# Kernel optimization log

Measured on AMD Instinct MI355X. Metric: run time of the kernel, lower is better.

Reference implementation:

```python
import jax, jax.numpy as jnp
import numpy as np

DIM = 512
HEADS = 8
DIM_HEAD = 64
INNER = HEADS * DIM_HEAD  # 512
EPS = 1e-6


def setup_inputs() -> dict:
    key = jax.random.key(0)
    ks = jax.random.split(key, 6)
    B, N = 8, 2048
    x = jax.random.normal(ks[0], (B, N, DIM), dtype=jnp.float32)
    # nn.Linear stores weight as [out, in]; we keep that layout and transpose in matmul.
    w_qkv = jax.random.normal(ks[1], (3 * INNER, DIM), dtype=jnp.float32) * (1.0 / np.sqrt(DIM))
    w_proj = jax.random.normal(ks[2], (DIM, INNER), dtype=jnp.float32) * (1.0 / np.sqrt(INNER))
    b_proj = jax.random.normal(ks[3], (DIM,), dtype=jnp.float32) * 0.01
    ln_gamma = jnp.ones((DIM,), dtype=jnp.float32)
    ln_beta = jnp.zeros((DIM,), dtype=jnp.float32)
    return {"x": x, "w_qkv": w_qkv, "w_proj": w_proj, "b_proj": b_proj,
            "ln_gamma": ln_gamma, "ln_beta": ln_beta}


def reference(x, w_qkv, w_proj, b_proj, ln_gamma, ln_beta):
    B, N, D = x.shape
    H, Dh = HEADS, DIM_HEAD
    # LayerNorm (eps=1e-6)
    mu = jnp.mean(x, axis=-1, keepdims=True)
    var = jnp.mean(jnp.square(x - mu), axis=-1, keepdims=True)
    xn = (x - mu) * jax.lax.rsqrt(var + EPS) * ln_gamma + ln_beta
    # QKV projection (no bias)
    qkv = xn @ w_qkv.T  # [B, N, 3*INNER]
    q, k, v = jnp.split(qkv, 3, axis=-1)
    # [B, N, H, Dh] -> [B, H, N, Dh]
    q = q.reshape(B, N, H, Dh).transpose(0, 2, 1, 3)
    k = k.reshape(B, N, H, Dh).transpose(0, 2, 1, 3)
    v = v.reshape(B, N, H, Dh).transpose(0, 2, 1, 3)
    scale = Dh ** (-0.5)
    attn = jnp.einsum('bhnd,bhmd->bhnm', q, k) * scale  # [B, H, N, N]
    attn = jax.nn.softmax(attn, axis=-1)
    out = jnp.einsum('bhnm,bhmd->bhnd', attn, v)  # [B, H, N, Dh]
    out = out.transpose(0, 2, 1, 3).reshape(B, N, H * Dh)
    out = out @ w_proj.T + b_proj
    return out
```

## Files before the change

kernel.cpp:

```cpp
#include <hip/hip_runtime.h>

typedef unsigned short u16;
typedef __bf16 bf16x8 __attribute__((ext_vector_type(8)));
typedef float f32x4 __attribute__((ext_vector_type(4)));

#define DIMD 512
#define SEQN 2048
#define NB   8
#define NH   8
#define DH   64
#define BHN  (NB*NH)
#define MROWS (NB*SEQN)
#define QSCALE 0.18033688f

__device__ __forceinline__ u16 f2bf(float f) {
  union { float f; unsigned u; } x; x.f = f;
  unsigned r = x.u + 0x7fffu + ((x.u >> 16) & 1u);
  return (u16)(r >> 16);
}
__device__ __forceinline__ u16 f2bf_fast(float f) {
  union { float f; unsigned u; } x; x.f = f;
  return (u16)((x.u + 0x8000u) >> 16);
}

__device__ __forceinline__ void gll16(const u16* g, u16* lbase) {
#if __has_builtin(__builtin_amdgcn_global_load_lds)
  __builtin_amdgcn_global_load_lds(
      (const __attribute__((address_space(1))) unsigned int*)g,
      (__attribute__((address_space(3))) unsigned int*)lbase, 16, 0, 0);
#else
  *(uint4*)((u16*)lbase + (threadIdx.x & 63) * 8) = *(const uint4*)g;
#endif
}

__global__ __launch_bounds__(256) void wcvt(const float* __restrict__ w,
                                            u16* __restrict__ o, int n) {
  int i = (blockIdx.x * 256 + threadIdx.x) * 8;
  if (i >= n) return;
  float4 f0 = *(const float4*)(w + i);
  float4 f1 = *(const float4*)(w + i + 4);
  union { uint4 v; u16 s[8]; } u;
  u.s[0] = f2bf(f0.x); u.s[1] = f2bf(f0.y); u.s[2] = f2bf(f0.z); u.s[3] = f2bf(f0.w);
  u.s[4] = f2bf(f1.x); u.s[5] = f2bf(f1.y); u.s[6] = f2bf(f1.z); u.s[7] = f2bf(f1.w);
  *(uint4*)(o + i) = u.v;
}

__global__ __launch_bounds__(256) void ln_kernel(
    const float* __restrict__ x, const float* __restrict__ gamma,
    const float* __restrict__ beta, u16* __restrict__ xn) {
  int row = blockIdx.x * 4 + (threadIdx.x >> 6);
  int lane = threadIdx.x & 63;
  const float* xr = x + (size_t)row * DIMD;
  float f[8], g[8], b[8];
  *(float4*)&f[0] = *(const float4*)(xr + lane * 8);
  *(float4*)&f[4] = *(const float4*)(xr + lane * 8 + 4);
  *(float4*)&g[0] = *(const float4*)(gamma + lane * 8);
  *(float4*)&g[4] = *(const float4*)(gamma + lane * 8 + 4);
  *(float4*)&b[0] = *(const float4*)(beta + lane * 8);
  *(float4*)&b[4] = *(const float4*)(beta + lane * 8 + 4);
  float sum = 0.f, sq = 0.f;
#pragma unroll
  for (int i = 0; i < 8; ++i) { sum += f[i]; sq += f[i] * f[i]; }
#pragma unroll
  for (int off = 1; off < 64; off <<= 1) {
    sum += __shfl_xor(sum, off, 64);
    sq  += __shfl_xor(sq, off, 64);
  }
  float mean = sum * (1.0f / DIMD);
  float var = sq * (1.0f / DIMD) - mean * mean;
  float rstd = rsqrtf(var + 1e-6f);
  union { uint4 v; u16 s[8]; } uo;
#pragma unroll
  for (int i = 0; i < 8; ++i)
    uo.s[i] = f2bf((f[i] - mean) * rstd * g[i] + b[i]);
  *(uint4*)(xn + (size_t)row * DIMD + lane * 8) = uo.v;
}

__global__ __launch_bounds__(256) void qkv_gemm(
    const u16* __restrict__ A, const u16* __restrict__ Bm,
    u16* __restrict__ qo, u16* __restrict__ ko, u16* __restrict__ vto) {
  __shared__ __align__(16) u16 la[128 * 32];
  __shared__ __align__(16) u16 lb[128 * 32];
  const int K = DIMD;
  int tid = threadIdx.x;
  int bm = blockIdx.x, bn = blockIdx.y;
  int wid = tid >> 6, lane = tid & 63, lm = lane & 15, quad = lane >> 4;
  int wm = wid >> 1, wn = wid & 1;
  f32x4 acc[4][4] = {};
  const u16* Ab = A + (size_t)(bm * 128) * K;
  const u16* Bb = Bm + (size_t)(bn * 128) * K;
  int srow = (lane >> 2), scol = (lane & 3) * 8;
  for (int k0 = 0; k0 < K; k0 += 32) {
    __syncthreads();
#pragma unroll
    for (int r = 0; r < 2; ++r) {
      int seg = wid * 2 + r;
      int row = seg * 16 + srow;
      gll16(Ab + (size_t)row * K + k0 + scol, &la[seg * 512]);
      gll16(Bb + (size_t)row * K + k0 + scol, &lb[seg * 512]);
    }
    __syncthreads();
    bf16x8 af[4], bfr[4];
#pragma unroll
    for (int i = 0; i < 4; ++i)
      af[i] = *(const bf16x8*)&la[(wm * 64 + i * 16 + lm) * 32 + quad * 8];
#pragma unroll
    for (int j = 0; j < 4; ++j)
      bfr[j] = *(const bf16x8*)&lb[(wn * 64 + j * 16 + lm) * 32 + quad * 8];
#pragma unroll
    for (int i = 0; i < 4; ++i)
#pragma unroll
      for (int j = 0; j < 4; ++j)
        acc[i][j] = __builtin_amdgcn_mfma_f32_16x16x32_bf16(af[i], bfr[j], acc[i][j], 0, 0, 0);
  }
#pragma unroll
  for (int i = 0; i < 4; ++i) {
#pragma unroll
    for (int j = 0; j < 4; ++j) {
      int col = bn * 128 + wn * 64 + j * 16 + lm;
      int part = col >> 9, rem = col & 511;
      int h = rem >> 6, d = rem & 63;
      float sc = (part == 0) ? QSCALE : 1.0f;
#pragma unroll
      for (int r = 0; r < 4; ++r) {
        int rg = bm * 128 + wm * 64 + i * 16 + quad * 4 + r;
        int b = rg >> 11, nn = rg & 2047;
        int bh = b * NH + h;
        u16 val = f2bf(acc[i][j][r] * sc);
        if (part == 0)      qo[((size_t)bh * SEQN + nn) * DH + d] = val;
        else if (part == 1) ko[((size_t)bh * SEQN + nn) * DH + d] = val;
        else                vto[((size_t)bh * DH + d) * SEQN + nn] = val;
      }
    }
  }
}

__global__ __launch_bounds__(256, 4) void attn_kernel(
    const u16* __restrict__ q, const u16* __restrict__ k,
    const u16* __restrict__ vt, u16* __restrict__ att) {
  __shared__ __align__(16) u16 kt[64 * 64];
  __shared__ __align__(16) u16 vtt[64 * 64];
  __shared__ __align__(16) u16 plds[4 * 2 * 1152];
  int bh = blockIdx.x;
  int wid = threadIdx.x >> 6, lane = threadIdx.x & 63;
  int lm = lane & 15, quad = lane >> 4;
  int qrow0 = blockIdx.y * 128 + wid * 32;
  const u16* qb = q + (size_t)bh * SEQN * DH;
  const u16* kb = k + (size_t)bh * SEQN * DH;
  const u16* vb = vt + (size_t)bh * DH * SEQN;

  int cb_row = lane >> 3, cb_sub = lane & 7;
  int xsw = quad ^ (lm & 7);

  bf16x8 qf[2][2];
#pragma unroll
  for (int g = 0; g < 2; ++g)
#pragma unroll
    for (int c = 0; c < 2; ++c)
      qf[g][c] = *(const bf16x8*)(qb + (size_t)(qrow0 + g * 16 + lm) * DH + c * 32 + quad * 8);

  f32x4 Ot[2][4] = {};
  f32x4 lv[2] = {};

  for (int j0 = 0; j0 < SEQN; j0 += 64) {
    __syncthreads();
    if (wid < 2) {
#pragma unroll
      for (int i = 0; i < 4; ++i) {
        int rbase = wid * 32 + i * 8;
        int row = rbase + cb_row;
        int sc = ((cb_sub ^ (row & 7)) * 8);
        gll16(kb + (size_t)(j0 + row) * DH + sc, &kt[(wid * 256 + i * 64) * 8]);
      }
    } else {
#pragma unroll
      for (int i = 0; i < 4; ++i) {
        int rbase = (wid - 2) * 32 + i * 8;
        int row = rbase + cb_row;
        int sc = ((cb_sub ^ (row & 7)) * 8);
        gll16(vb + (size_t)row * SEQN + j0 + sc, &vtt[((wid - 2) * 256 + i * 64) * 8]);
      }
    }
    __syncthreads();

    bf16x8 kf[4][2];
#pragma unroll
    for (int js = 0; js < 4; ++js) {
      int row = js * 16 + lm;
      kf[js][0] = *(const bf16x8*)&kt[row * 64 + xsw * 8];
      kf[js][1] = *(const bf16x8*)&kt[row * 64 + (xsw ^ 4) * 8];
    }
    bf16x8 pa[2][2];
#pragma unroll
    for (int g = 0; g < 2; ++g) {
      u16* pg = plds + (wid * 2 + g) * 1152;
#pragma unroll
      for (int js = 0; js < 4; ++js) {
        f32x4 z = {0.f, 0.f, 0.f, 0.f};
        z = __builtin_amdgcn_mfma_f32_16x16x32_bf16(kf[js][0], qf[g][0], z, 0, 0, 0);
        z = __builtin_amdgcn_mfma_f32_16x16x32_bf16(kf[js][1], qf[g][1], z, 0, 0, 0);
        union { unsigned long long ll; u16 s4[4]; } pk;
#pragma unroll
        for (int r = 0; r < 4; ++r) {
          float p = __builtin_amdgcn_exp2f(z[r]);
          lv[g][r] += p;
          pk.s4[r] = f2bf_fast(p);
        }
        *(unsigned long long*)&pg[lm * 72 + js * 16 + quad * 4] = pk.ll;
      }
      pa[g][0] = *(const bf16x8*)&pg[lm * 72 + quad * 8];
      pa[g][1] = *(const bf16x8*)&pg[lm * 72 + 32 + quad * 8];
    }
#pragma unroll
    for (int db = 0; db < 4; ++db) {
      int row = db * 16 + lm;
      bf16x8 va0 = *(const bf16x8*)&vtt[row * 64 + xsw * 8];
      bf16x8 va1 = *(const bf16x8*)&vtt[row * 64 + (xsw ^ 4) * 8];
      Ot[0][db] = __builtin_amdgcn_mfma_f32_16x16x32_bf16(va0, pa[0][0], Ot[0][db], 0, 0, 0);
      Ot[0][db] = __builtin_amdgcn_mfma_f32_16x16x32_bf16(va1, pa[0][1], Ot[0][db], 0, 0, 0);
      Ot[1][db] = __builtin_amdgcn_mfma_f32_16x16x32_bf16(va0, pa[1][0], Ot[1][db], 0, 0, 0);
      Ot[1][db] = __builtin_amdgcn_mfma_f32_16x16x32_bf16(va1, pa[1][1], Ot[1][db], 0, 0, 0);
    }
  }
  int b = bh >> 3, h = bh & 7;
#pragma unroll
  for (int g = 0; g < 2; ++g) {
    float rs = (lv[g][0] + lv[g][1]) + (lv[g][2] + lv[g][3]);
    rs += __shfl_xor(rs, 16, 64);
    rs += __shfl_xor(rs, 32, 64);
    float inv = 1.0f / rs;
    size_t rowoff = ((size_t)(b * SEQN + qrow0 + g * 16 + lm)) * DIMD + h * DH;
#pragma unroll
    for (int db = 0; db < 4; ++db) {
      union { unsigned long long ll; u16 s4[4]; } ok;
#pragma unroll
      for (int r = 0; r < 4; ++r) ok.s4[r] = f2bf(Ot[g][db][r] * inv);
      *(unsigned long long*)&att[rowoff + db * 16 + quad * 4] = ok.ll;
    }
  }
}

__global__ __launch_bounds__(256) void proj_gemm(
    const u16* __restrict__ A, const u16* __restrict__ Bm,
    const float* __restrict__ bias, float* __restrict__ C) {
  __shared__ __align__(16) u16 la[128 * 32];
  __shared__ __align__(16) u16 lb[128 * 32];
  const int K = DIMD, N = DIMD;
  int tid = threadIdx.x;
  int bm = blockIdx.x, bn = blockIdx.y;
  int wid = tid >> 6, lane = tid & 63, lm = lane & 15, quad = lane >> 4;
  int wm = wid >> 1, wn = wid & 1;
  f32x4 acc[4][4] = {};
  const u16* Ab = A + (size_t)(bm * 128) * K;
  const u16* Bb = Bm + (size_t)(bn * 128) * K;
  int srow = (lane >> 2), scol = (lane & 3) * 8;
  for (int k0 = 0; k0 < K; k0 += 32) {
    __syncthreads();
#pragma unroll
    for (int r = 0; r < 2; ++r) {
      int seg = wid * 2 + r;
      int row = seg * 16 + srow;
      gll16(Ab + (size_t)row * K + k0 + scol, &la[seg * 512]);
      gll16(Bb + (size_t)row * K + k0 + scol, &lb[seg * 512]);
    }
    __syncthreads();
    bf16x8 af[4], bfr[4];
#pragma unroll
    for (int i = 0; i < 4; ++i)
      af[i] = *(const bf16x8*)&la[(wm * 64 + i * 16 + lm) * 32 + quad * 8];
#pragma unroll
    for (int j = 0; j < 4; ++j)
      bfr[j] = *(const bf16x8*)&lb[(wn * 64 + j * 16 + lm) * 32 + quad * 8];
#pragma unroll
    for (int i = 0; i < 4; ++i)
#pragma unroll
      for (int j = 0; j < 4; ++j)
        acc[i][j] = __builtin_amdgcn_mfma_f32_16x16x32_bf16(af[i], bfr[j], acc[i][j], 0, 0, 0);
  }
#pragma unroll
  for (int i = 0; i < 4; ++i)
#pragma unroll
    for (int j = 0; j < 4; ++j) {
      int col = bn * 128 + wn * 64 + j * 16 + lm;
      float bv = bias[col];
#pragma unroll
      for (int r = 0; r < 4; ++r) {
        int rg = bm * 128 + wm * 64 + i * 16 + quad * 4 + r;
        C[(size_t)rg * N + col] = acc[i][j][r] + bv;
      }
    }
}

extern "C" void kernel_launch(void* const* d_in, const int* in_sizes, int n_in,
                              void* d_out, int out_size, void* d_ws, size_t ws_size,
                              hipStream_t stream) {
  const float* x      = (const float*)d_in[0];
  const float* w_qkv  = (const float*)d_in[1];
  const float* w_proj = (const float*)d_in[2];
  const float* b_proj = (const float*)d_in[3];
  const float* gamma  = (const float*)d_in[4];
  const float* beta   = (const float*)d_in[5];
  float* out = (float*)d_out;

  const size_t SZ = (size_t)MROWS * DIMD;
  u16* xn  = (u16*)d_ws;
  u16* q   = xn + SZ;
  u16* kk  = q + SZ;
  u16* vt  = kk + SZ;
  u16* wqb = vt + SZ;
  u16* wpb = wqb + (size_t)3 * DIMD * DIMD;
  u16* att = xn;

  const int NQKV = 3 * DIMD * DIMD;
  const int NPRJ = DIMD * DIMD;
  wcvt<<<dim3(NQKV / 2048), dim3(256), 0, stream>>>(w_qkv, wqb, NQKV);
  wcvt<<<dim3(NPRJ / 2048), dim3(256), 0, stream>>>(w_proj, wpb, NPRJ);
  ln_kernel<<<dim3(MROWS / 4), dim3(256), 0, stream>>>(x, gamma, beta, xn);
  qkv_gemm<<<dim3(MROWS / 128, (3 * DIMD) / 128), dim3(256), 0, stream>>>(
      xn, wqb, q, kk, vt);
  attn_kernel<<<dim3(BHN, SEQN / 128), dim3(256), 0, stream>>>(q, kk, vt, att);
  proj_gemm<<<dim3(MROWS / 128, DIMD / 128), dim3(256), 0, stream>>>(
      att, wpb, b_proj, out);
}
```

Baseline: 255.2 us.

## Double-buffer attention K/V tiles, merge weight casts, vectorize V-transpose stores

The attention kernel now double-buffers the K and V^T LDS tiles, issuing the next tile's global-to-LDS loads right after a single barrier so they overlap with the current tile's MFMA work. The per-wave P scratch shrinks to one buffer, and the occupancy hint drops from 4 to 3 blocks per CU to make room for the larger LDS footprint. The QKV GEMM epilogue is split by the block's output part, so V^T writes go out as packed 64-bit stores and the scale select leaves the inner loop. The two weight-conversion launches are merged into one kernel to save a launch.

```diff
diff --git a/kernel.cpp b/kernel.cpp
--- a/kernel.cpp
+++ b/kernel.cpp
@@ -33,16 +33,19 @@
 #endif
 }
 
-__global__ __launch_bounds__(256) void wcvt(const float* __restrict__ w,
-                                            u16* __restrict__ o, int n) {
+__global__ __launch_bounds__(256) void wcvt2(
+    const float* __restrict__ wa, const float* __restrict__ wb,
+    u16* __restrict__ oa, u16* __restrict__ ob, int na, int nb) {
   int i = (blockIdx.x * 256 + threadIdx.x) * 8;
-  if (i >= n) return;
-  float4 f0 = *(const float4*)(w + i);
-  float4 f1 = *(const float4*)(w + i + 4);
+  const float* src; u16* dst; int idx;
+  if (i < na) { src = wa; dst = oa; idx = i; }
+  else { idx = i - na; if (idx >= nb) return; src = wb; dst = ob; }
+  float4 f0 = *(const float4*)(src + idx);
+  float4 f1 = *(const float4*)(src + idx + 4);
   union { uint4 v; u16 s[8]; } u;
   u.s[0] = f2bf(f0.x); u.s[1] = f2bf(f0.y); u.s[2] = f2bf(f0.z); u.s[3] = f2bf(f0.w);
   u.s[4] = f2bf(f1.x); u.s[5] = f2bf(f1.y); u.s[6] = f2bf(f1.z); u.s[7] = f2bf(f1.w);
-  *(uint4*)(o + i) = u.v;
+  *(uint4*)(dst + idx) = u.v;
 }
 
 __global__ __launch_bounds__(256) void ln_kernel(
@@ -113,34 +116,46 @@
       for (int j = 0; j < 4; ++j)
         acc[i][j] = __builtin_amdgcn_mfma_f32_16x16x32_bf16(af[i], bfr[j], acc[i][j], 0, 0, 0);
   }
-#pragma unroll
-  for (int i = 0; i < 4; ++i) {
-#pragma unroll
-    for (int j = 0; j < 4; ++j) {
-      int col = bn * 128 + wn * 64 + j * 16 + lm;
-      int part = col >> 9, rem = col & 511;
-      int h = rem >> 6, d = rem & 63;
-      float sc = (part == 0) ? QSCALE : 1.0f;
-#pragma unroll
-      for (int r = 0; r < 4; ++r) {
-        int rg = bm * 128 + wm * 64 + i * 16 + quad * 4 + r;
+  int part = bn >> 2;
+  if (part == 2) {
+#pragma unroll
+    for (int i = 0; i < 4; ++i)
+#pragma unroll
+      for (int j = 0; j < 4; ++j) {
+        int col = bn * 128 + wn * 64 + j * 16 + lm;
+        int rem = col & 511, h = rem >> 6, d = rem & 63;
+        int rg = bm * 128 + wm * 64 + i * 16 + quad * 4;
         int b = rg >> 11, nn = rg & 2047;
-        int bh = b * NH + h;
-        u16 val = f2bf(acc[i][j][r] * sc);
-        if (part == 0)      qo[((size_t)bh * SEQN + nn) * DH + d] = val;
-        else if (part == 1) ko[((size_t)bh * SEQN + nn) * DH + d] = val;
-        else                vto[((size_t)bh * DH + d) * SEQN + nn] = val;
-      }
-    }
-  }
-}
-
-__global__ __launch_bounds__(256, 4) void attn_kernel(
+        union { unsigned long long ll; u16 s4[4]; } pk;
+#pragma unroll
+        for (int r = 0; r < 4; ++r) pk.s4[r] = f2bf(acc[i][j][r]);
+        *(unsigned long long*)&vto[((size_t)(b * NH + h) * DH + d) * SEQN + nn] = pk.ll;
+      }
+  } else {
+    u16* dst = part ? ko : qo;
+    float sc = part ? 1.0f : QSCALE;
+#pragma unroll
+    for (int i = 0; i < 4; ++i)
+#pragma unroll
+      for (int j = 0; j < 4; ++j) {
+        int col = bn * 128 + wn * 64 + j * 16 + lm;
+        int rem = col & 511, h = rem >> 6, d = rem & 63;
+#pragma unroll
+        for (int r = 0; r < 4; ++r) {
+          int rg = bm * 128 + wm * 64 + i * 16 + quad * 4 + r;
+          int b = rg >> 11, nn = rg & 2047;
+          dst[((size_t)(b * NH + h) * SEQN + nn) * DH + d] = f2bf(acc[i][j][r] * sc);
+        }
+      }
+  }
+}
+
+__global__ __launch_bounds__(256, 3) void attn_kernel(
     const u16* __restrict__ q, const u16* __restrict__ k,
     const u16* __restrict__ vt, u16* __restrict__ att) {
-  __shared__ __align__(16) u16 kt[64 * 64];
-  __shared__ __align__(16) u16 vtt[64 * 64];
-  __shared__ __align__(16) u16 plds[4 * 2 * 1152];
+  __shared__ __align__(16) u16 kt[2][64 * 64];
+  __shared__ __align__(16) u16 vtt[2][64 * 64];
+  __shared__ __align__(16) u16 plds[4 * 16 * 72];
   int bh = blockIdx.x;
   int wid = threadIdx.x >> 6, lane = threadIdx.x & 63;
   int lm = lane & 15, quad = lane >> 4;
@@ -148,6 +163,7 @@
   const u16* qb = q + (size_t)bh * SEQN * DH;
   const u16* kb = k + (size_t)bh * SEQN * DH;
   const u16* vb = vt + (size_t)bh * DH * SEQN;
+  u16* pw = plds + wid * (16 * 72);
 
   int cb_row = lane >> 3, cb_sub = lane & 7;
   int xsw = quad ^ (lm & 7);
@@ -162,38 +178,40 @@
   f32x4 Ot[2][4] = {};
   f32x4 lv[2] = {};
 
-  for (int j0 = 0; j0 < SEQN; j0 += 64) {
-    __syncthreads();
+  auto stage = [&](int bsel, int j0) {
     if (wid < 2) {
 #pragma unroll
       for (int i = 0; i < 4; ++i) {
-        int rbase = wid * 32 + i * 8;
-        int row = rbase + cb_row;
-        int sc = ((cb_sub ^ (row & 7)) * 8);
-        gll16(kb + (size_t)(j0 + row) * DH + sc, &kt[(wid * 256 + i * 64) * 8]);
+        int row = wid * 32 + i * 8 + cb_row;
+        int sc = (cb_sub ^ (row & 7)) * 8;
+        gll16(kb + (size_t)(j0 + row) * DH + sc, &kt[bsel][wid * 2048 + i * 512]);
       }
     } else {
 #pragma unroll
       for (int i = 0; i < 4; ++i) {
-        int rbase = (wid - 2) * 32 + i * 8;
-        int row = rbase + cb_row;
-        int sc = ((cb_sub ^ (row & 7)) * 8);
-        gll16(vb + (size_t)row * SEQN + j0 + sc, &vtt[((wid - 2) * 256 + i * 64) * 8]);
-      }
-    }
-    __syncthreads();
+        int row = (wid - 2) * 32 + i * 8 + cb_row;
+        int sc = (cb_sub ^ (row & 7)) * 8;
+        gll16(vb + (size_t)row * SEQN + j0 + sc, &vtt[bsel][(wid - 2) * 2048 + i * 512]);
+      }
+    }
+  };
+
+  stage(0, 0);
+  for (int t = 0; t < SEQN / 64; ++t) {
+    int bsel = t & 1;
+    __syncthreads();
+    if (t + 1 < SEQN / 64) stage(bsel ^ 1, (t + 1) * 64);
 
     bf16x8 kf[4][2];
 #pragma unroll
     for (int js = 0; js < 4; ++js) {
       int row = js * 16 + lm;
-      kf[js][0] = *(const bf16x8*)&kt[row * 64 + xsw * 8];
-      kf[js][1] = *(const bf16x8*)&kt[row * 64 + (xsw ^ 4) * 8];
+      kf[js][0] = *(const bf16x8*)&kt[bsel][row * 64 + xsw * 8];
+      kf[js][1] = *(const bf16x8*)&kt[bsel][row * 64 + (xsw ^ 4) * 8];
     }
     bf16x8 pa[2][2];
 #pragma unroll
     for (int g = 0; g < 2; ++g) {
-      u16* pg = plds + (wid * 2 + g) * 1152;
 #pragma unroll
       for (int js = 0; js < 4; ++js) {
         f32x4 z = {0.f, 0.f, 0.f, 0.f};
@@ -206,16 +224,16 @@
           lv[g][r] += p;
           pk.s4[r] = f2bf_fast(p);
         }
-        *(unsigned long long*)&pg[lm * 72 + js * 16 + quad * 4] = pk.ll;
-      }
-      pa[g][0] = *(const bf16x8*)&pg[lm * 72 + quad * 8];
-      pa[g][1] = *(const bf16x8*)&pg[lm * 72 + 32 + quad * 8];
+        *(unsigned long long*)&pw[lm * 72 + js * 16 + quad * 4] = pk.ll;
+      }
+      pa[g][0] = *(const bf16x8*)&pw[lm * 72 + quad * 8];
+      pa[g][1] = *(const bf16x8*)&pw[lm * 72 + 32 + quad * 8];
     }
 #pragma unroll
     for (int db = 0; db < 4; ++db) {
       int row = db * 16 + lm;
-      bf16x8 va0 = *(const bf16x8*)&vtt[row * 64 + xsw * 8];
-      bf16x8 va1 = *(const bf16x8*)&vtt[row * 64 + (xsw ^ 4) * 8];
+      bf16x8 va0 = *(const bf16x8*)&vtt[bsel][row * 64 + xsw * 8];
+      bf16x8 va1 = *(const bf16x8*)&vtt[bsel][row * 64 + (xsw ^ 4) * 8];
       Ot[0][db] = __builtin_amdgcn_mfma_f32_16x16x32_bf16(va0, pa[0][0], Ot[0][db], 0, 0, 0);
       Ot[0][db] = __builtin_amdgcn_mfma_f32_16x16x32_bf16(va1, pa[0][1], Ot[0][db], 0, 0, 0);
       Ot[1][db] = __builtin_amdgcn_mfma_f32_16x16x32_bf16(va0, pa[1][0], Ot[1][db], 0, 0, 0);
@@ -313,8 +331,8 @@
 
   const int NQKV = 3 * DIMD * DIMD;
   const int NPRJ = DIMD * DIMD;
-  wcvt<<<dim3(NQKV / 2048), dim3(256), 0, stream>>>(w_qkv, wqb, NQKV);
-  wcvt<<<dim3(NPRJ / 2048), dim3(256), 0, stream>>>(w_proj, wpb, NPRJ);
+  wcvt2<<<dim3((NQKV + NPRJ) / 2048), dim3(256), 0, stream>>>(
+      w_qkv, w_proj, wqb, wpb, NQKV, NPRJ);
   ln_kernel<<<dim3(MROWS / 4), dim3(256), 0, stream>>>(x, gamma, beta, xn);
   qkv_gemm<<<dim3(MROWS / 128, (3 * DIMD) / 128), dim3(256), 0, stream>>>(
       xn, wqb, q, kk, vt);
```

Measured after the change: 236.5 us. 7.3% less time.
